# Performance work log

Hardware: AMD Instinct MI355X
Metric: run time of the kernel (lower is better)

## Reference

```python
import jax, jax.numpy as jnp
import numpy as np

B, D, H = 4096, 512, 16
WRITE_TAU = 0.3

def setup_inputs() -> dict:
    key = jax.random.key(0)
    ks = jax.random.split(key, 8)
    s = 1.0 / np.sqrt(D)
    return {
        "z_query": jax.random.normal(ks[0], (B, D), dtype=jnp.float32),
        "z_state": jax.random.normal(ks[1], (B, D), dtype=jnp.float32),
        "z_value": jax.random.normal(ks[2], (B, D), dtype=jnp.float32),
        "confidence": jax.random.uniform(ks[3], (B,), dtype=jnp.float32),
        "Wk": jax.random.normal(ks[4], (D, H * D), dtype=jnp.float32) * s,  # key_proj weight (in, out)
        "Wv": jax.random.normal(ks[5], (D, H * D), dtype=jnp.float32) * s,  # val_proj weight
        "Wo": jax.random.normal(ks[6], (D, D), dtype=jnp.float32) * s,      # out_proj weight
        "memory": jax.random.normal(ks[7], (H, D, D), dtype=jnp.float32) * 0.02,  # M buffer (nonzero for testing)
    }

def reference(z_query, z_state, z_value, confidence, Wk, Wv, Wo, memory):
    # ---- read: v_ret = out_proj(mean_h(M_h @ k_h)) ----
    k = (z_query @ Wk).reshape(B, H, D)                 # (B,H,d)
    v = jnp.einsum('bhd,hde->bhe', k, jax.lax.stop_gradient(memory))
    v_ret = v.mean(axis=1) @ Wo                          # (B,d)

    # ---- write (no-grad in original): masked outer-product accumulation ----
    lam = jnp.clip(1.0 - confidence, 0.0, 1.0)           # (B,)
    mask = (lam > WRITE_TAU).astype(z_state.dtype)       # (B,)
    lam_m = lam * mask                                   # zero out non-surprising rows
    kw = (z_state @ Wk).reshape(B, H, D)
    vw = (z_value @ Wv).reshape(B, H, D)
    delta = jnp.einsum('bhd,bhe,b->hde', kw, vw, lam_m)  # (H,d,d)
    new_memory = memory + delta / (mask.sum() + 1e-6)
    new_memory = jax.lax.stop_gradient(new_memory)

    return v_ret, new_memory
```

## Files before the change

### kernel.cpp

```cpp
#include <hip/hip_runtime.h>

typedef unsigned short u16;
typedef __attribute__((ext_vector_type(8))) short bf16x8;
typedef __attribute__((ext_vector_type(4))) float f32x4;

#define B_DIM 4096
#define D_DIM 512
#define H_DIM 16

typedef const __attribute__((address_space(1))) unsigned int* gas_t;
typedef __attribute__((address_space(3))) unsigned int* las_t;

__device__ __forceinline__ u16 f2bf(float f) {
  union { float f; unsigned u; } x;
  x.f = f;
  unsigned r = x.u + 0x7FFFu + ((x.u >> 16) & 1u);
  return (u16)(r >> 16);
}

__device__ __forceinline__ uint4 pack8(float4 v0, float4 v1) {
  union { uint4 q; u16 h[8]; } u;
  u.h[0] = f2bf(v0.x); u.h[1] = f2bf(v0.y); u.h[2] = f2bf(v0.z); u.h[3] = f2bf(v0.w);
  u.h[4] = f2bf(v1.x); u.h[5] = f2bf(v1.y); u.h[6] = f2bf(v1.z); u.h[7] = f2bf(v1.w);
  return u.q;
}

struct TJob {
  const float* in;
  void* out;
  void* out2;
  const float* conf;
  int rows, cols, tiles_x, tile_off, kind;
};
struct TJobs { TJob j[9]; };

__global__ __launch_bounds__(256) void mega_prep(TJobs J, float* __restrict__ countp) {
  __shared__ float tile[64][65];
  __shared__ float wsum[4];
  const int tid = threadIdx.x;
  int b = blockIdx.x;
  int sel = 0;
#pragma unroll
  for (int i = 1; i < 9; ++i)
    if (b >= J.j[i].tile_off) sel = i;
  TJob jb = J.j[sel];
  b -= jb.tile_off;

  if (jb.kind == 3) {
    long long base = (long long)b * 4096 + tid * 16;
    float4 z = {0.f, 0.f, 0.f, 0.f};
    float* o = (float*)jb.out + base;
    *(float4*)o = z; *(float4*)(o + 4) = z; *(float4*)(o + 8) = z; *(float4*)(o + 12) = z;
    return;
  }
  if (jb.kind == 2) {
    float m = 0.f;
    for (int i = tid; i < B_DIM; i += 256) {
      float l = 1.0f - jb.in[i];
      l = fminf(fmaxf(l, 0.f), 1.f);
      m += (l > 0.3f) ? 1.f : 0.f;
    }
    for (int off = 32; off; off >>= 1) m += __shfl_down(m, off, 64);
    if ((tid & 63) == 0) wsum[tid >> 6] = m;
    __syncthreads();
    if (tid == 0) countp[0] = wsum[0] + wsum[1] + wsum[2] + wsum[3];
    return;
  }

  const long long c0 = (long long)(b % jb.tiles_x) * 64;
  const long long r0 = (long long)(b / jb.tiles_x) * 64;
  const int rr = tid >> 4;
  const int cc4 = (tid & 15) * 4;
#pragma unroll
  for (int i = 0; i < 4; ++i) {
    int row = i * 16 + rr;
    float4 v = *(const float4*)(jb.in + (r0 + row) * jb.cols + c0 + cc4);
    if (jb.kind == 1) {
      float l = 1.0f - jb.conf[r0 + row];
      l = fminf(fmaxf(l, 0.f), 1.f);
      float s = (l > 0.3f) ? l : 0.f;
      v.x *= s; v.y *= s; v.z *= s; v.w *= s;
    }
    tile[row][cc4] = v.x; tile[row][cc4 + 1] = v.y;
    tile[row][cc4 + 2] = v.z; tile[row][cc4 + 3] = v.w;
    if (jb.out2) {
      union { uint2 u; u16 h[4]; } p;
      p.h[0] = f2bf(v.x); p.h[1] = f2bf(v.y); p.h[2] = f2bf(v.z); p.h[3] = f2bf(v.w);
      *(uint2*)((u16*)jb.out2 + (r0 + row) * jb.cols + c0 + cc4) = p.u;
    }
  }
  __syncthreads();
  const int orow = tid >> 2;
  const int seg = tid & 3;
  union { uint4 q[2]; u16 h[16]; } o;
#pragma unroll
  for (int i = 0; i < 16; ++i) o.h[i] = f2bf(tile[seg * 16 + i][orow]);
  u16* outp = (u16*)jb.out + (c0 + orow) * jb.rows + r0 + seg * 16;
  *(uint4*)outp = o.q[0];
  *(uint4*)(outp + 8) = o.q[1];
}

struct GJob {
  const void* A; const void* Bp; void* C;
  const float* addsrc; const float* cnt;
  long long lda, ldb, ldc, sa_b, sb_b, sc_b, sadd_b;
  float alpha;
  int K, k_chunk, tm, tn, batched, mode, aflag, bflag, nblocks;
};
struct GJobs { GJob j[2]; };

__global__ __launch_bounds__(256, 2) void gemm128(GJobs JJ) {
  __shared__ alignas(16) u16 As[2][128 * 64];
  __shared__ alignas(16) u16 Bs[2][128 * 64];

  int b = blockIdx.x;
  GJob J = JJ.j[0];
  if (b >= J.nblocks) { b -= J.nblocks; J = JJ.j[1]; }

  const int tilesper = J.tm * J.tn;
  const int bz = b / tilesper;
  const int rel = b % tilesper;
  const long long m0 = (long long)(rel / J.tn) * 128;
  const long long n0 = (long long)(rel % J.tn) * 128;

  long long aoff = 0, boff = 0, coff = 0, doff = 0, k0 = 0;
  int Kl = J.K;
  if (J.batched) {
    aoff = (long long)bz * J.sa_b;
    boff = (long long)bz * J.sb_b;
    coff = (long long)bz * J.sc_b;
    doff = (long long)bz * J.sadd_b;
  } else {
    k0 = (long long)bz * J.k_chunk;
    Kl = J.k_chunk;
  }

  const int tid = threadIdx.x;
  const int lane = tid & 63, wave = tid >> 6;
  const int wm = (wave & 1) * 64, wn = (wave >> 1) * 64;
  const int fm = lane & 15, fg = lane >> 4;

  auto stage = [&](u16* dst, const void* src, long long ld, long long off,
                   long long rbase, long long t, int isf32) {
    if (!isf32) {
      const u16* gb = (const u16*)src + off;
#pragma unroll
      for (int j = 0; j < 4; ++j) {
        int cc = wave * 4 + j;
        int row = cc * 8 + (lane >> 3);
        int cg = (lane & 7) ^ (row & 7);
        const u16* g = gb + (rbase + row) * ld + t + cg * 8;
        __builtin_amdgcn_global_load_lds((gas_t)(const void*)g,
                                         (las_t)(void*)(dst + cc * 512 + lane * 8),
                                         16, 0, 0);
      }
    } else {
      const float* gb = (const float*)src + off;
#pragma unroll
      for (int p = 0; p < 4; ++p) {
        int idx = p * 256 + tid;
        int row = idx >> 3, cg = idx & 7;
        const float* g = gb + (rbase + row) * ld + t + cg * 8;
        float4 v0 = *(const float4*)g;
        float4 v1 = *(const float4*)(g + 4);
        *(uint4*)&dst[row * 64 + ((cg ^ (row & 7)) * 8)] = pack8(v0, v1);
      }
    }
  };

  f32x4 acc[4][4];
#pragma unroll
  for (int i = 0; i < 4; ++i)
#pragma unroll
    for (int j = 0; j < 4; ++j) acc[i][j] = (f32x4){0.f, 0.f, 0.f, 0.f};

  const int nIter = Kl >> 6;
  stage(As[0], J.A, J.lda, aoff, m0, k0, J.aflag);
  stage(Bs[0], J.Bp, J.ldb, boff, n0, k0, J.bflag);

  for (int i = 0; i < nIter; ++i) {
    __syncthreads();
    if (i + 1 < nIter) {
      long long t = k0 + (long long)(i + 1) * 64;
      stage(As[(i + 1) & 1], J.A, J.lda, aoff, m0, t, J.aflag);
      stage(Bs[(i + 1) & 1], J.Bp, J.ldb, boff, n0, t, J.bflag);
    }
    const u16* Ab = As[i & 1];
    const u16* Bb = Bs[i & 1];
#pragma unroll
    for (int kcc = 0; kcc < 8; kcc += 4) {
      bf16x8 af[4], bfr[4];
#pragma unroll
      for (int fi = 0; fi < 4; ++fi) {
        int row = wm + fi * 16 + fm;
        af[fi] = *(const bf16x8*)&Ab[row * 64 + (((kcc + fg) ^ (row & 7)) * 8)];
      }
#pragma unroll
      for (int fj = 0; fj < 4; ++fj) {
        int row = wn + fj * 16 + fm;
        bfr[fj] = *(const bf16x8*)&Bb[row * 64 + (((kcc + fg) ^ (row & 7)) * 8)];
      }
#pragma unroll
      for (int fi = 0; fi < 4; ++fi)
#pragma unroll
        for (int fj = 0; fj < 4; ++fj)
          acc[fi][fj] = __builtin_amdgcn_mfma_f32_16x16x32_bf16(af[fi], bfr[fj], acc[fi][fj], 0, 0, 0);
    }
  }

  float inv = (J.mode == 3) ? 1.0f / (*J.cnt + 1e-6f) : 0.0f;
#pragma unroll
  for (int fi = 0; fi < 4; ++fi) {
#pragma unroll
    for (int r = 0; r < 4; ++r) {
      long long row = m0 + wm + fi * 16 + fg * 4 + r;
#pragma unroll
      for (int fj = 0; fj < 4; ++fj) {
        long long col = n0 + wn + fj * 16 + fm;
        long long idx = row * J.ldc + col;
        float v = acc[fi][fj][r];
        if (J.mode == 0) {
          atomicAdd((float*)J.C + idx, v * J.alpha);
        } else if (J.mode == 1) {
          ((u16*)J.C)[coff + idx] = f2bf(v * J.alpha);
        } else if (J.mode == 2) {
          ((float*)J.C)[coff + idx] = v * J.alpha;
        } else {
          ((float*)J.C)[coff + idx] = J.addsrc[doff + idx] + v * inv;
        }
      }
    }
  }
}

extern "C" void kernel_launch(void* const* d_in, const int* in_sizes, int n_in,
                              void* d_out, int out_size, void* d_ws, size_t ws_size,
                              hipStream_t stream) {
  (void)in_sizes; (void)n_in; (void)out_size; (void)ws_size;
  const float* zq   = (const float*)d_in[0];
  const float* zs   = (const float*)d_in[1];
  const float* zv   = (const float*)d_in[2];
  const float* conf = (const float*)d_in[3];
  const float* Wk   = (const float*)d_in[4];
  const float* Wv   = (const float*)d_in[5];
  const float* Wo   = (const float*)d_in[6];
  const float* mem  = (const float*)d_in[7];

  float* vret = (float*)d_out;
  float* newmem = vret + (long long)B_DIM * D_DIM;

  float* count = (float*)d_ws;
  float* Pf = (float*)((char*)d_ws + 256);
  float* Sf = (float*)((char*)d_ws + 256 + 1048576);
  u16* bb   = (u16*)((char*)d_ws + 2097408);
  u16* zsT   = bb;
  u16* zvlT  = bb + 2097152;
  u16* WkT   = bb + 4194304;
  u16* WvT   = bb + 8388608;
  u16* memT  = bb + 12582912;
  u16* WoT   = bb + 16777216;
  u16* QT    = bb + 17039360;
  u16* UT    = bb + 17301504;
  u16* Wk_bf = bb + 21495808;

  TJobs T;
  T.j[0] = {zs,  zsT,  nullptr, nullptr, 4096, 512,  8,   0,    0};
  T.j[1] = {zv,  zvlT, nullptr, conf,    4096, 512,  8,   512,  1};
  T.j[2] = {Wk,  WkT,  Wk_bf,   nullptr, 512,  8192, 128, 1024, 0};
  T.j[3] = {Wv,  WvT,  nullptr, nullptr, 512,  8192, 128, 2048, 0};
  T.j[4] = {mem, memT, nullptr, nullptr, 8192, 512,  8,   3072, 0};
  T.j[5] = {Wo,  WoT,  nullptr, nullptr, 512,  512,  8,   4096, 0};
  T.j[6] = {nullptr, Pf, nullptr, nullptr, 0, 0, 0,      4160, 3};
  T.j[7] = {nullptr, Sf, nullptr, nullptr, 0, 0, 0,      4224, 3};
  T.j[8] = {conf, nullptr, nullptr, nullptr, 0, 0, 0,    4288, 2};
  mega_prep<<<4289, 256, 0, stream>>>(T, count);

  GJobs D2;
  D2.j[0] = {Wk_bf, memT, Pf, nullptr, nullptr,
             8192, 8192, 512, 0, 0, 0, 0,
             1.0f, 8192, 512, 4, 4, 0, 0, 0, 0, 256};
  D2.j[1] = {zsT, zvlT, Sf, nullptr, nullptr,
             4096, 4096, 512, 0, 0, 0, 0,
             1.0f, 4096, 512, 4, 4, 0, 0, 0, 0, 128};
  gemm128<<<384, 256, 0, stream>>>(D2);

  GJobs D3;
  D3.j[0] = {WvT, Sf, UT, nullptr, nullptr,
             512, 512, 512, 262144, 0, 262144, 0,
             1.0f, 512, 512, 4, 4, 1, 1, 0, 1, 256};
  D3.j[1] = {WoT, Pf, QT, nullptr, nullptr,
             512, 512, 512, 0, 0, 0, 0,
             1.0f / 16.0f, 512, 512, 4, 4, 0, 1, 0, 1, 16};
  gemm128<<<272, 256, 0, stream>>>(D3);

  GJobs D4;
  D4.j[0] = {WkT, UT, newmem, mem, count,
             512, 512, 512, 262144, 262144, 262144, 262144,
             1.0f, 512, 512, 4, 4, 1, 3, 0, 0, 256};
  D4.j[1] = {zq, QT, vret, nullptr, nullptr,
             512, 512, 512, 0, 0, 0, 0,
             1.0f, 512, 512, 32, 4, 0, 2, 1, 0, 128};
  gemm128<<<384, 256, 0, stream>>>(D4);
}
```

Baseline: 218.2 us.

## Replace split-K float atomics with stacked bf16 partials and a reduction pass

The split-K GEMMs that built P and S used fp32 atomicAdd into zeroed buffers. They now write each K-chunk's partial as bf16 into stacked buffers, and a new mega_prep job sums the partials into bf16 reduced matrices. This removes the atomics and the zero-fill jobs, and the downstream GEMMs read bf16 inputs instead of fp32. The cost is an extra kernel launch, extra partial-buffer traffic, and lower precision from rounding the partials to bf16.

Result: faster. 208.0 us (-4.7%).

```diff
diff --git a/kernel.cpp b/kernel.cpp
--- a/kernel.cpp
+++ b/kernel.cpp
@@ -2,6 +2,7 @@
 
 typedef unsigned short u16;
 typedef __attribute__((ext_vector_type(8))) short bf16x8;
+typedef __attribute__((ext_vector_type(8))) unsigned short u16x8;
 typedef __attribute__((ext_vector_type(4))) float f32x4;
 
 #define B_DIM 4096
@@ -16,6 +17,12 @@
   x.f = f;
   unsigned r = x.u + 0x7FFFu + ((x.u >> 16) & 1u);
   return (u16)(r >> 16);
+}
+
+__device__ __forceinline__ float bf2f(u16 h) {
+  union { unsigned u; float f; } x;
+  x.u = ((unsigned)h) << 16;
+  return x.f;
 }
 
 __device__ __forceinline__ uint4 pack8(float4 v0, float4 v1) {
@@ -32,7 +39,7 @@
   const float* conf;
   int rows, cols, tiles_x, tile_off, kind;
 };
-struct TJobs { TJob j[9]; };
+struct TJobs { TJob j[8]; };
 
 __global__ __launch_bounds__(256) void mega_prep(TJobs J, float* __restrict__ countp) {
   __shared__ float tile[64][65];
@@ -41,16 +48,28 @@
   int b = blockIdx.x;
   int sel = 0;
 #pragma unroll
-  for (int i = 1; i < 9; ++i)
+  for (int i = 1; i < 8; ++i)
     if (b >= J.j[i].tile_off) sel = i;
   TJob jb = J.j[sel];
   b -= jb.tile_off;
 
   if (jb.kind == 3) {
-    long long base = (long long)b * 4096 + tid * 16;
-    float4 z = {0.f, 0.f, 0.f, 0.f};
-    float* o = (float*)jb.out + base;
-    *(float4*)o = z; *(float4*)(o + 4) = z; *(float4*)(o + 8) = z; *(float4*)(o + 12) = z;
+    const u16* src = (const u16*)jb.in;
+    u16* dst = (u16*)jb.out;
+    const int nsum = jb.rows;
+    const long long incols = jb.cols;
+    const long long r = (long long)b * 4 + (tid >> 6);
+    const int c = (tid & 63) * 8;
+    float acc[8] = {0.f, 0.f, 0.f, 0.f, 0.f, 0.f, 0.f, 0.f};
+    for (int s = 0; s < nsum; ++s) {
+      u16x8 v = *(const u16x8*)(src + r * incols + s * 512 + c);
+#pragma unroll
+      for (int i = 0; i < 8; ++i) acc[i] += bf2f(v[i]);
+    }
+    union { uint4 q; u16 h[8]; } o;
+#pragma unroll
+    for (int i = 0; i < 8; ++i) o.h[i] = f2bf(acc[i]);
+    *(uint4*)(dst + r * 512 + c) = o.q;
     return;
   }
   if (jb.kind == 2) {
@@ -133,6 +152,7 @@
   } else {
     k0 = (long long)bz * J.k_chunk;
     Kl = J.k_chunk;
+    coff = (long long)bz * J.sc_b;
   }
 
   const int tid = threadIdx.x;
@@ -219,9 +239,7 @@
         long long col = n0 + wn + fj * 16 + fm;
         long long idx = row * J.ldc + col;
         float v = acc[fi][fj][r];
-        if (J.mode == 0) {
-          atomicAdd((float*)J.C + idx, v * J.alpha);
-        } else if (J.mode == 1) {
+        if (J.mode == 1) {
           ((u16*)J.C)[coff + idx] = f2bf(v * J.alpha);
         } else if (J.mode == 2) {
           ((float*)J.C)[coff + idx] = v * J.alpha;
@@ -250,18 +268,20 @@
   float* newmem = vret + (long long)B_DIM * D_DIM;
 
   float* count = (float*)d_ws;
-  float* Pf = (float*)((char*)d_ws + 256);
-  float* Sf = (float*)((char*)d_ws + 256 + 1048576);
-  u16* bb   = (u16*)((char*)d_ws + 2097408);
+  u16* bb = (u16*)((char*)d_ws + 256);
   u16* zsT   = bb;
   u16* zvlT  = bb + 2097152;
   u16* WkT   = bb + 4194304;
   u16* WvT   = bb + 8388608;
   u16* memT  = bb + 12582912;
   u16* WoT   = bb + 16777216;
-  u16* QT    = bb + 17039360;
-  u16* UT    = bb + 17301504;
-  u16* Wk_bf = bb + 21495808;
+  u16* Wk_bf = bb + 17039360;
+  u16* Pstk  = bb + 21233664;
+  u16* Sstk  = bb + 25427968;
+  u16* Pred  = bb + 27525120;
+  u16* Sred  = bb + 27787264;
+  u16* QT    = bb + 28049408;
+  u16* UT    = bb + 28311552;
 
   TJobs T;
   T.j[0] = {zs,  zsT,  nullptr, nullptr, 4096, 512,  8,   0,    0};
@@ -270,27 +290,37 @@
   T.j[3] = {Wv,  WvT,  nullptr, nullptr, 512,  8192, 128, 2048, 0};
   T.j[4] = {mem, memT, nullptr, nullptr, 8192, 512,  8,   3072, 0};
   T.j[5] = {Wo,  WoT,  nullptr, nullptr, 512,  512,  8,   4096, 0};
-  T.j[6] = {nullptr, Pf, nullptr, nullptr, 0, 0, 0,      4160, 3};
-  T.j[7] = {nullptr, Sf, nullptr, nullptr, 0, 0, 0,      4224, 3};
-  T.j[8] = {conf, nullptr, nullptr, nullptr, 0, 0, 0,    4288, 2};
-  mega_prep<<<4289, 256, 0, stream>>>(T, count);
+  T.j[6] = {conf, nullptr, nullptr, nullptr, 0, 0, 0,     4160, 2};
+  T.j[7] = {nullptr, nullptr, nullptr, nullptr, 0, 0, 0, 1 << 30, 0};
+  mega_prep<<<4161, 256, 0, stream>>>(T, count);
 
   GJobs D2;
-  D2.j[0] = {Wk_bf, memT, Pf, nullptr, nullptr,
-             8192, 8192, 512, 0, 0, 0, 0,
-             1.0f, 8192, 512, 4, 4, 0, 0, 0, 0, 256};
-  D2.j[1] = {zsT, zvlT, Sf, nullptr, nullptr,
-             4096, 4096, 512, 0, 0, 0, 0,
-             1.0f, 4096, 512, 4, 4, 0, 0, 0, 0, 128};
+  D2.j[0] = {Wk_bf, memT, Pstk, nullptr, nullptr,
+             8192, 8192, 8192, 0, 0, 512, 0,
+             1.0f, 8192, 512, 4, 4, 0, 1, 0, 0, 256};
+  D2.j[1] = {zsT, zvlT, Sstk, nullptr, nullptr,
+             4096, 4096, 4096, 0, 0, 512, 0,
+             1.0f, 4096, 512, 4, 4, 0, 1, 0, 0, 128};
   gemm128<<<384, 256, 0, stream>>>(D2);
 
+  TJobs R;
+  R.j[0] = {(const float*)Pstk, Pred, nullptr, nullptr, 16, 8192, 0, 0,   3};
+  R.j[1] = {(const float*)Sstk, Sred, nullptr, nullptr, 8,  4096, 0, 128, 3};
+  R.j[2] = {nullptr, nullptr, nullptr, nullptr, 0, 0, 0, 1 << 30, 0};
+  R.j[3] = {nullptr, nullptr, nullptr, nullptr, 0, 0, 0, 1 << 30, 0};
+  R.j[4] = {nullptr, nullptr, nullptr, nullptr, 0, 0, 0, 1 << 30, 0};
+  R.j[5] = {nullptr, nullptr, nullptr, nullptr, 0, 0, 0, 1 << 30, 0};
+  R.j[6] = {nullptr, nullptr, nullptr, nullptr, 0, 0, 0, 1 << 30, 0};
+  R.j[7] = {nullptr, nullptr, nullptr, nullptr, 0, 0, 0, 1 << 30, 0};
+  mega_prep<<<256, 256, 0, stream>>>(R, count);
+
   GJobs D3;
-  D3.j[0] = {WvT, Sf, UT, nullptr, nullptr,
+  D3.j[0] = {WvT, Sred, UT, nullptr, nullptr,
              512, 512, 512, 262144, 0, 262144, 0,
-             1.0f, 512, 512, 4, 4, 1, 1, 0, 1, 256};
-  D3.j[1] = {WoT, Pf, QT, nullptr, nullptr,
+             1.0f, 512, 512, 4, 4, 1, 1, 0, 0, 256};
+  D3.j[1] = {WoT, Pred, QT, nullptr, nullptr,
              512, 512, 512, 0, 0, 0, 0,
-             1.0f / 16.0f, 512, 512, 4, 4, 0, 1, 0, 1, 16};
+             1.0f / 16.0f, 512, 512, 4, 4, 0, 1, 0, 0, 16};
   gemm128<<<272, 256, 0, stream>>>(D3);
 
   GJobs D4;
```
